# Optimization experiments

Hardware: AMD Instinct MI355X
Metric: run time of the kernel (lower is better)

## Reference

```python
import jax, jax.numpy as jnp
import numpy as np

N_NODES = 50000
N_EDGES = 800000
FEAT_DIM = 1024
EMBED_DIM = 128


def setup_inputs() -> dict:
    key = jax.random.key(0)
    k_x, k_w, k_r, k_c, k_v = jax.random.split(key, 5)
    x = jax.random.normal(k_x, (N_NODES, FEAT_DIM), dtype=jnp.float32)
    # xavier-uniform equivalent for weight [embed_dim, feat_dim]
    limit = float(np.sqrt(6.0 / (EMBED_DIM + FEAT_DIM)))
    weight = jax.random.uniform(k_w, (EMBED_DIM, FEAT_DIM), dtype=jnp.float32,
                                minval=-limit, maxval=limit)
    # sparse adjacency in COO form (row = destination, col = source)
    adj_row = jax.random.randint(k_r, (N_EDGES,), 0, N_NODES, dtype=jnp.int32)
    adj_col = jax.random.randint(k_c, (N_EDGES,), 0, N_NODES, dtype=jnp.int32)
    adj_vals = jax.random.uniform(k_v, (N_EDGES,), dtype=jnp.float32)
    return {"x": x, "weight": weight, "adj_row": adj_row,
            "adj_col": adj_col, "adj_vals": adj_vals}


def reference(x, weight, adj_row, adj_col, adj_vals):
    # Fused GeMM-SpMM: out = A @ (x @ W^T)
    h = jnp.einsum('nf,ef->ne', x, weight)          # [N, embed_dim] dense GEMM
    msgs = adj_vals[:, None] * h[adj_col]           # gather source rows, scale by edge weight
    out = jax.ops.segment_sum(msgs, adj_row, num_segments=N_NODES)  # scatter-add to dest rows
    return out
```

## Files before the change

kernel.cpp:

```cpp
#include <hip/hip_runtime.h>
#include <hip/hip_bf16.h>

#define FEAT 1024
#define EMBED 128
#define CAP 64
#define OVF_CAP 4096

typedef __attribute__((ext_vector_type(8))) short short8;
typedef __attribute__((ext_vector_type(4))) float floatx4;

__device__ inline ushort f2bf(float f) {
    __hip_bfloat16 h = __float2bfloat16(f);
    return *reinterpret_cast<ushort*>(&h);
}
__device__ inline float bfbits_lo(uint u) {
    uint v = u << 16; return *reinterpret_cast<float*>(&v);
}
__device__ inline float bfbits_hi(uint u) {
    uint v = u & 0xffff0000u; return *reinterpret_cast<float*>(&v);
}

__device__ inline void async_copy16(const void* g, void* l) {
    __builtin_amdgcn_global_load_lds(
        (const __attribute__((address_space(1))) void*)g,
        (__attribute__((address_space(3))) void*)l, 16, 0, 0);
}

__global__ void swizzle_weight_kernel(const float* __restrict__ w,
                                      ushort* __restrict__ wbs) {
    int gid = blockIdx.x * blockDim.x + threadIdx.x;
    int l = gid & 63;
    int t = (gid >> 6) & 7;
    int s = gid >> 9;
    int row = t * 16 + (l & 15);
    int col = s * 32 + (l >> 4) * 8;
    const float* src = w + (size_t)row * FEAT + col;
    float4 v0 = *(const float4*)(src);
    float4 v1 = *(const float4*)(src + 4);
    short8 o;
    o[0] = f2bf(v0.x); o[1] = f2bf(v0.y); o[2] = f2bf(v0.z); o[3] = f2bf(v0.w);
    o[4] = f2bf(v1.x); o[5] = f2bf(v1.y); o[6] = f2bf(v1.z); o[7] = f2bf(v1.w);
    *(short8*)(wbs + (size_t)gid * 8) = o;
}

__launch_bounds__(256, 2)
__global__ void gemm_xwT_kernel(const float* __restrict__ x,
                                const ushort* __restrict__ wbs,
                                ushort* __restrict__ hb, int n_nodes) {
    __shared__ ushort lds[2][16384];

    const int lane = threadIdx.x & 63;
    const int wave = threadIdx.x >> 6;
    const int q    = lane >> 4;
    const int m    = lane & 15;
    const int base = blockIdx.x * 128 + wave * 32;

    int row0 = base + m;
    int row1 = base + 16 + m;
    int r0l = row0 < n_nodes ? row0 : (n_nodes - 1);
    int r1l = row1 < n_nodes ? row1 : (n_nodes - 1);
    const float* xp0 = x + (size_t)r0l * FEAT + q * 8;
    const float* xp1 = x + (size_t)r1l * FEAT + q * 8;

    const char* wb = (const char*)wbs;
    const size_t stage_src_off = (size_t)(wave * 8 * 64 + lane) * 16;
    const int    stage_dst_off = wave * 8192;

    {
        const char* src = wb + stage_src_off;
        char* dst = (char*)lds[0] + stage_dst_off;
#pragma unroll
        for (int k = 0; k < 8; ++k)
            async_copy16(src + k * 1024, dst + k * 1024);
    }

    float4 A[4][4];
#pragma unroll
    for (int u = 0; u < 4; ++u) {
        A[u][0] = *(const float4*)(xp0 + u * 32);
        A[u][1] = *(const float4*)(xp0 + u * 32 + 4);
        A[u][2] = *(const float4*)(xp1 + u * 32);
        A[u][3] = *(const float4*)(xp1 + u * 32 + 4);
    }

    floatx4 acc[2][8];
#pragma unroll
    for (int rf = 0; rf < 2; ++rf)
#pragma unroll
        for (int t = 0; t < 8; ++t) acc[rf][t] = (floatx4)(0.0f);

    __syncthreads();

    for (int c = 0; c < 8; ++c) {
        const ushort* buf = lds[c & 1];
        if (c < 7) {
            const char* src = wb + (size_t)(c + 1) * 32768 + stage_src_off;
            char* dst = (char*)lds[(c + 1) & 1] + stage_dst_off;
#pragma unroll
            for (int k = 0; k < 8; ++k)
                async_copy16(src + k * 1024, dst + k * 1024);
        }
#pragma unroll
        for (int u = 0; u < 4; ++u) {
            const ushort* bs = buf + u * 4096 + lane * 8;
            short8 bf[8];
#pragma unroll
            for (int t = 0; t < 8; ++t) bf[t] = *(const short8*)(bs + t * 512);

            short8 af0, af1;
            af0[0] = f2bf(A[u][0].x); af0[1] = f2bf(A[u][0].y);
            af0[2] = f2bf(A[u][0].z); af0[3] = f2bf(A[u][0].w);
            af0[4] = f2bf(A[u][1].x); af0[5] = f2bf(A[u][1].y);
            af0[6] = f2bf(A[u][1].z); af0[7] = f2bf(A[u][1].w);
            af1[0] = f2bf(A[u][2].x); af1[1] = f2bf(A[u][2].y);
            af1[2] = f2bf(A[u][2].z); af1[3] = f2bf(A[u][2].w);
            af1[4] = f2bf(A[u][3].x); af1[5] = f2bf(A[u][3].y);
            af1[6] = f2bf(A[u][3].z); af1[7] = f2bf(A[u][3].w);

            if (u == 3 && c < 7) {
                const float* p0 = xp0 + (c + 1) * 128;
                const float* p1 = xp1 + (c + 1) * 128;
#pragma unroll
                for (int uu = 0; uu < 4; ++uu) {
                    A[uu][0] = *(const float4*)(p0 + uu * 32);
                    A[uu][1] = *(const float4*)(p0 + uu * 32 + 4);
                    A[uu][2] = *(const float4*)(p1 + uu * 32);
                    A[uu][3] = *(const float4*)(p1 + uu * 32 + 4);
                }
            }
#pragma unroll
            for (int t = 0; t < 8; ++t) {
                acc[0][t] = __builtin_amdgcn_mfma_f32_16x16x32_bf16(af0, bf[t], acc[0][t], 0, 0, 0);
                acc[1][t] = __builtin_amdgcn_mfma_f32_16x16x32_bf16(af1, bf[t], acc[1][t], 0, 0, 0);
            }
        }
        __syncthreads();
    }

#pragma unroll
    for (int rf = 0; rf < 2; ++rf) {
#pragma unroll
        for (int t = 0; t < 8; ++t) {
#pragma unroll
            for (int r = 0; r < 4; ++r) {
                int rr = base + rf * 16 + q * 4 + r;
                if (rr < n_nodes)
                    hb[(size_t)rr * EMBED + t * 16 + m] = f2bf(acc[rf][t][r]);
            }
        }
    }
}

__global__ void bucket_fill_kernel(const int* __restrict__ adj_row,
                                   const int* __restrict__ adj_col,
                                   const float* __restrict__ adj_vals,
                                   int* __restrict__ cnt,
                                   int2* __restrict__ bucket,
                                   int* __restrict__ ovf_cnt,
                                   int* __restrict__ ovf_list,
                                   int n_edges) {
    int e = blockIdx.x * blockDim.x + threadIdx.x;
    if (e >= n_edges) return;
    int r = adj_row[e];
    int slot = atomicAdd(&cnt[r], 1);
    if (slot < CAP) {
        bucket[(size_t)r * CAP + slot] = make_int2(adj_col[e], __float_as_int(adj_vals[e]));
    } else {
        int oi = atomicAdd(ovf_cnt, 1);
        if (oi < OVF_CAP) ovf_list[oi] = e;
    }
}

__launch_bounds__(256)
__global__ void gather_kernel(const int* __restrict__ cnt,
                              const int2* __restrict__ bucket,
                              const ushort* __restrict__ hb,
                              float* __restrict__ out, int n_nodes) {
    int node = __builtin_amdgcn_readfirstlane(blockIdx.x * 4 + (threadIdx.x >> 6));
    if (node >= n_nodes) return;
    int lane = threadIdx.x & 63;
    int c = cnt[node];
    if (c > CAP) c = CAP;
    const int2* bp = bucket + (size_t)node * CAP;
    const ushort* hl = hb + lane * 2;

    float accx = 0.0f, accy = 0.0f;
    int j = 0;
    for (; j + 8 <= c; j += 8) {
        int4 e01 = *(const int4*)(bp + j);
        int4 e23 = *(const int4*)(bp + j + 2);
        int4 e45 = *(const int4*)(bp + j + 4);
        int4 e67 = *(const int4*)(bp + j + 6);
        uint u0 = *(const uint*)(hl + (size_t)e01.x * EMBED);
        uint u1 = *(const uint*)(hl + (size_t)e01.z * EMBED);
        uint u2 = *(const uint*)(hl + (size_t)e23.x * EMBED);
        uint u3 = *(const uint*)(hl + (size_t)e23.z * EMBED);
        uint u4 = *(const uint*)(hl + (size_t)e45.x * EMBED);
        uint u5 = *(const uint*)(hl + (size_t)e45.z * EMBED);
        uint u6 = *(const uint*)(hl + (size_t)e67.x * EMBED);
        uint u7 = *(const uint*)(hl + (size_t)e67.z * EMBED);
        float w0 = __int_as_float(e01.y), w1 = __int_as_float(e01.w);
        float w2 = __int_as_float(e23.y), w3 = __int_as_float(e23.w);
        float w4 = __int_as_float(e45.y), w5 = __int_as_float(e45.w);
        float w6 = __int_as_float(e67.y), w7 = __int_as_float(e67.w);
        accx = fmaf(w0, bfbits_lo(u0), accx);  accy = fmaf(w0, bfbits_hi(u0), accy);
        accx = fmaf(w1, bfbits_lo(u1), accx);  accy = fmaf(w1, bfbits_hi(u1), accy);
        accx = fmaf(w2, bfbits_lo(u2), accx);  accy = fmaf(w2, bfbits_hi(u2), accy);
        accx = fmaf(w3, bfbits_lo(u3), accx);  accy = fmaf(w3, bfbits_hi(u3), accy);
        accx = fmaf(w4, bfbits_lo(u4), accx);  accy = fmaf(w4, bfbits_hi(u4), accy);
        accx = fmaf(w5, bfbits_lo(u5), accx);  accy = fmaf(w5, bfbits_hi(u5), accy);
        accx = fmaf(w6, bfbits_lo(u6), accx);  accy = fmaf(w6, bfbits_hi(u6), accy);
        accx = fmaf(w7, bfbits_lo(u7), accx);  accy = fmaf(w7, bfbits_hi(u7), accy);
    }
    for (; j + 2 <= c; j += 2) {
        int4 e01 = *(const int4*)(bp + j);
        uint u0 = *(const uint*)(hl + (size_t)e01.x * EMBED);
        uint u1 = *(const uint*)(hl + (size_t)e01.z * EMBED);
        float w0 = __int_as_float(e01.y), w1 = __int_as_float(e01.w);
        accx = fmaf(w0, bfbits_lo(u0), accx);  accy = fmaf(w0, bfbits_hi(u0), accy);
        accx = fmaf(w1, bfbits_lo(u1), accx);  accy = fmaf(w1, bfbits_hi(u1), accy);
    }
    if (j < c) {
        int2 ev = bp[j];
        uint u = *(const uint*)(hl + (size_t)ev.x * EMBED);
        float w = __int_as_float(ev.y);
        accx = fmaf(w, bfbits_lo(u), accx);
        accy = fmaf(w, bfbits_hi(u), accy);
    }
    *(float2*)(out + (size_t)node * EMBED + lane * 2) = make_float2(accx, accy);
}

__global__ void overflow_fixup_kernel(const int* __restrict__ ovf_cnt,
                                      const int* __restrict__ ovf_list,
                                      const int* __restrict__ adj_row,
                                      const int* __restrict__ adj_col,
                                      const float* __restrict__ adj_vals,
                                      const ushort* __restrict__ hb,
                                      float* __restrict__ out) {
    int n = *ovf_cnt;
    if (n > OVF_CAP) n = OVF_CAP;
    int f = threadIdx.x;
    for (int i = blockIdx.x; i < n; i += gridDim.x) {
        int e = ovf_list[i];
        uint us = hb[(size_t)adj_col[e] * EMBED + f];
        uint v = us << 16;
        atomicAdd(&out[(size_t)adj_row[e] * EMBED + f],
                  adj_vals[e] * *reinterpret_cast<float*>(&v));
    }
}

extern "C" void kernel_launch(void* const* d_in, const int* in_sizes, int n_in,
                              void* d_out, int out_size, void* d_ws, size_t ws_size,
                              hipStream_t stream) {
    const float* x        = (const float*)d_in[0];
    const float* w        = (const float*)d_in[1];
    const int*   adj_row  = (const int*)d_in[2];
    const int*   adj_col  = (const int*)d_in[3];
    const float* adj_vals = (const float*)d_in[4];

    const int n_nodes = in_sizes[0] / FEAT;
    const int n_edges = in_sizes[2];
    float* out = (float*)d_out;

    char* ws = (char*)d_ws;
    ushort* wbs = (ushort*)ws;
    size_t off = 262144;
    ushort* hb = (ushort*)(ws + off);
    off += (size_t)n_nodes * EMBED * sizeof(ushort);
    char* meta = ws + off;
    int* cnt      = (int*)meta;
    int* ovf_cnt  = (int*)(meta + (size_t)n_nodes * 4);
    int* ovf_list = ovf_cnt + 1;
    size_t meta_bytes = ((size_t)n_nodes * 4 + 4 + OVF_CAP * 4 + 15) & ~(size_t)15;
    int2* bucket = (int2*)(meta + meta_bytes);

    hipMemsetAsync(meta, 0, meta_bytes, stream);

    swizzle_weight_kernel<<<64, 256, 0, stream>>>(w, wbs);

    gemm_xwT_kernel<<<(n_nodes + 127) / 128, 256, 0, stream>>>(x, wbs, hb, n_nodes);

    bucket_fill_kernel<<<(n_edges + 255) / 256, 256, 0, stream>>>(
        adj_row, adj_col, adj_vals, cnt, bucket, ovf_cnt, ovf_list, n_edges);

    gather_kernel<<<(n_nodes + 3) / 4, 256, 0, stream>>>(cnt, bucket, hb, out, n_nodes);

    overflow_fixup_kernel<<<64, 128, 0, stream>>>(
        ovf_cnt, ovf_list, adj_row, adj_col, adj_vals, hb, out);
}
```

Before: 390.8 us.

## Fuse bucket fill into GEMM launch and fold overflow fixup into gather

Runs the COO bucket fill as extra blocks of the GEMM kernel so the edge binning overlaps the dense GEMM. The separate overflow atomic kernel is removed; gather handles overflow edges inline for nodes whose count exceeds the cap. The x prefetch for the next chunk is split across two sub-steps to spread register pressure and load issue. This cuts two launches and the serialization between them, but bucket blocks share the LDS allocation and launch bounds of the GEMM blocks, and the inline overflow scan is linear in the overflow count.

Result: faster. 365.9 us (-6.4%).

```diff
diff --git a/kernel.cpp b/kernel.cpp
--- a/kernel.cpp
+++ b/kernel.cpp
@@ -44,10 +44,34 @@
 }
 
 __launch_bounds__(256, 2)
-__global__ void gemm_xwT_kernel(const float* __restrict__ x,
-                                const ushort* __restrict__ wbs,
-                                ushort* __restrict__ hb, int n_nodes) {
+__global__ void gemm_bucket_kernel(const float* __restrict__ x,
+                                   const ushort* __restrict__ wbs,
+                                   ushort* __restrict__ hb, int n_nodes,
+                                   const int* __restrict__ adj_row,
+                                   const int* __restrict__ adj_col,
+                                   const float* __restrict__ adj_vals,
+                                   int* __restrict__ cnt,
+                                   int2* __restrict__ bucket,
+                                   int* __restrict__ ovf_cnt,
+                                   int* __restrict__ ovf_list,
+                                   int n_edges, int gemm_blocks) {
     __shared__ ushort lds[2][16384];
+
+    if (blockIdx.x >= gemm_blocks) {
+        int e = (blockIdx.x - gemm_blocks) * 256 + threadIdx.x;
+        if (e < n_edges) {
+            int r = adj_row[e];
+            int slot = atomicAdd(&cnt[r], 1);
+            if (slot < CAP) {
+                bucket[(size_t)r * CAP + slot] =
+                    make_int2(adj_col[e], __float_as_int(adj_vals[e]));
+            } else {
+                int oi = atomicAdd(ovf_cnt, 1);
+                if (oi < OVF_CAP) ovf_list[oi] = e;
+            }
+        }
+        return;
+    }
 
     const int lane = threadIdx.x & 63;
     const int wave = threadIdx.x >> 6;
@@ -117,15 +141,25 @@
             af1[4] = f2bf(A[u][3].x); af1[5] = f2bf(A[u][3].y);
             af1[6] = f2bf(A[u][3].z); af1[7] = f2bf(A[u][3].w);
 
-            if (u == 3 && c < 7) {
+            if (c < 7) {
                 const float* p0 = xp0 + (c + 1) * 128;
                 const float* p1 = xp1 + (c + 1) * 128;
-#pragma unroll
-                for (int uu = 0; uu < 4; ++uu) {
-                    A[uu][0] = *(const float4*)(p0 + uu * 32);
-                    A[uu][1] = *(const float4*)(p0 + uu * 32 + 4);
-                    A[uu][2] = *(const float4*)(p1 + uu * 32);
-                    A[uu][3] = *(const float4*)(p1 + uu * 32 + 4);
+                if (u == 1) {
+#pragma unroll
+                    for (int uu = 0; uu < 2; ++uu) {
+                        A[uu][0] = *(const float4*)(p0 + uu * 32);
+                        A[uu][1] = *(const float4*)(p0 + uu * 32 + 4);
+                        A[uu][2] = *(const float4*)(p1 + uu * 32);
+                        A[uu][3] = *(const float4*)(p1 + uu * 32 + 4);
+                    }
+                } else if (u == 3) {
+#pragma unroll
+                    for (int uu = 2; uu < 4; ++uu) {
+                        A[uu][0] = *(const float4*)(p0 + uu * 32);
+                        A[uu][1] = *(const float4*)(p0 + uu * 32 + 4);
+                        A[uu][2] = *(const float4*)(p1 + uu * 32);
+                        A[uu][3] = *(const float4*)(p1 + uu * 32 + 4);
+                    }
                 }
             }
 #pragma unroll
@@ -151,36 +185,21 @@
     }
 }
 
-__global__ void bucket_fill_kernel(const int* __restrict__ adj_row,
-                                   const int* __restrict__ adj_col,
-                                   const float* __restrict__ adj_vals,
-                                   int* __restrict__ cnt,
-                                   int2* __restrict__ bucket,
-                                   int* __restrict__ ovf_cnt,
-                                   int* __restrict__ ovf_list,
-                                   int n_edges) {
-    int e = blockIdx.x * blockDim.x + threadIdx.x;
-    if (e >= n_edges) return;
-    int r = adj_row[e];
-    int slot = atomicAdd(&cnt[r], 1);
-    if (slot < CAP) {
-        bucket[(size_t)r * CAP + slot] = make_int2(adj_col[e], __float_as_int(adj_vals[e]));
-    } else {
-        int oi = atomicAdd(ovf_cnt, 1);
-        if (oi < OVF_CAP) ovf_list[oi] = e;
-    }
-}
-
 __launch_bounds__(256)
 __global__ void gather_kernel(const int* __restrict__ cnt,
                               const int2* __restrict__ bucket,
                               const ushort* __restrict__ hb,
+                              const int* __restrict__ ovf_cnt,
+                              const int* __restrict__ ovf_list,
+                              const int* __restrict__ adj_row,
+                              const int* __restrict__ adj_col,
+                              const float* __restrict__ adj_vals,
                               float* __restrict__ out, int n_nodes) {
     int node = __builtin_amdgcn_readfirstlane(blockIdx.x * 4 + (threadIdx.x >> 6));
     if (node >= n_nodes) return;
     int lane = threadIdx.x & 63;
-    int c = cnt[node];
-    if (c > CAP) c = CAP;
+    int c_raw = cnt[node];
+    int c = c_raw > CAP ? CAP : c_raw;
     const int2* bp = bucket + (size_t)node * CAP;
     const ushort* hl = hb + lane * 2;
 
@@ -227,26 +246,20 @@
         accx = fmaf(w, bfbits_lo(u), accx);
         accy = fmaf(w, bfbits_hi(u), accy);
     }
+    if (c_raw > CAP) {
+        int n = *ovf_cnt;
+        if (n > OVF_CAP) n = OVF_CAP;
+        for (int i = 0; i < n; ++i) {
+            int e = ovf_list[i];
+            if (adj_row[e] == node) {
+                uint u = *(const uint*)(hl + (size_t)adj_col[e] * EMBED);
+                float w = adj_vals[e];
+                accx = fmaf(w, bfbits_lo(u), accx);
+                accy = fmaf(w, bfbits_hi(u), accy);
+            }
+        }
+    }
     *(float2*)(out + (size_t)node * EMBED + lane * 2) = make_float2(accx, accy);
-}
-
-__global__ void overflow_fixup_kernel(const int* __restrict__ ovf_cnt,
-                                      const int* __restrict__ ovf_list,
-                                      const int* __restrict__ adj_row,
-                                      const int* __restrict__ adj_col,
-                                      const float* __restrict__ adj_vals,
-                                      const ushort* __restrict__ hb,
-                                      float* __restrict__ out) {
-    int n = *ovf_cnt;
-    if (n > OVF_CAP) n = OVF_CAP;
-    int f = threadIdx.x;
-    for (int i = blockIdx.x; i < n; i += gridDim.x) {
-        int e = ovf_list[i];
-        uint us = hb[(size_t)adj_col[e] * EMBED + f];
-        uint v = us << 16;
-        atomicAdd(&out[(size_t)adj_row[e] * EMBED + f],
-                  adj_vals[e] * *reinterpret_cast<float*>(&v));
-    }
 }
 
 extern "C" void kernel_launch(void* const* d_in, const int* in_sizes, int n_in,
@@ -278,13 +291,14 @@
 
     swizzle_weight_kernel<<<64, 256, 0, stream>>>(w, wbs);
 
-    gemm_xwT_kernel<<<(n_nodes + 127) / 128, 256, 0, stream>>>(x, wbs, hb, n_nodes);
-
-    bucket_fill_kernel<<<(n_edges + 255) / 256, 256, 0, stream>>>(
-        adj_row, adj_col, adj_vals, cnt, bucket, ovf_cnt, ovf_list, n_edges);
-
-    gather_kernel<<<(n_nodes + 3) / 4, 256, 0, stream>>>(cnt, bucket, hb, out, n_nodes);
-
-    overflow_fixup_kernel<<<64, 128, 0, stream>>>(
-        ovf_cnt, ovf_list, adj_row, adj_col, adj_vals, hb, out);
-}
+    const int gemm_blocks   = (n_nodes + 127) / 128;
+    const int bucket_blocks = (n_edges + 255) / 256;
+    gemm_bucket_kernel<<<gemm_blocks + bucket_blocks, 256, 0, stream>>>(
+        x, wbs, hb, n_nodes,
+        adj_row, adj_col, adj_vals,
+        cnt, bucket, ovf_cnt, ovf_list, n_edges, gemm_blocks);
+
+    gather_kernel<<<(n_nodes + 3) / 4, 256, 0, stream>>>(
+        cnt, bucket, hb, ovf_cnt, ovf_list, adj_row, adj_col, adj_vals,
+        out, n_nodes);
+}
```
